# Kernel tuning notes

Hardware: AMD Instinct MI355X
Metric: run time of the kernel (lower is better)

Reference implementation:

```python
import jax, jax.numpy as jnp
import numpy as np


def setup_inputs() -> dict:
    key = jax.random.key(0)
    ks = jax.random.split(key, 8)
    B, T, C, W, H = 2, 8, 64, 32, 32
    NOBJ, DIM = 4, 64
    s = 0.05
    return {
        "inputs": jax.random.normal(ks[0], (B, T, C, W, H), jnp.float32),
        "dyn_feat_inputs": jax.random.normal(ks[1], (B, NOBJ, T, C, W, H), jnp.float32),
        "wq": jax.random.normal(ks[2], (C // 2, C), jnp.float32) * s,
        "bq": jax.random.normal(ks[3], (C // 2,), jnp.float32) * s,
        "wk": jax.random.normal(ks[4], (C // 2, C), jnp.float32) * s,
        "bk": jax.random.normal(ks[5], (C // 2,), jnp.float32) * s,
        "wv": jax.random.normal(ks[6], (DIM, C), jnp.float32) * s,
        "bv": jax.random.normal(ks[7], (DIM,), jnp.float32) * s,
    }


def reference(inputs, dyn_feat_inputs, wq, bq, wk, bk, wv, bv):
    # inputs: [bs, T, ch, w, h]; dyn_feat_inputs: [bs, n_obj, T, ch, w, h]
    bs, T, ch, w, h = inputs.shape
    n_obj = dyn_feat_inputs.shape[1]
    N = w * h
    bsTO = bs * n_obj * T
    # repeat inputs across the object axis (broadcast, no copy until reshape)
    xin = jnp.broadcast_to(inputs[:, None], (bs, n_obj, T, ch, w, h)).reshape(bsTO, ch, N)
    xdyn = dyn_feat_inputs.reshape(bsTO, ch, N)
    # 1x1 convs == channel matmuls
    q = jnp.einsum('oc,bcn->bno', wq, xdyn) + bq            # [bsTO, N, ch//2]
    k = jnp.einsum('oc,bcn->bon', wk, xin) + bk[:, None]    # [bsTO, ch//2, N]
    energy = jnp.einsum('bno,bom->bnm', q, k)               # [bsTO, N, N] (NO scale, as in source)
    attn = jax.nn.softmax(energy, axis=-1)
    v = jnp.einsum('oc,bcn->bon', wv, xin) + bv[:, None]    # [bsTO, dim, N]
    # out = bmm(v, attn^T): out[b,d,m] = sum_n v[b,d,n] * attn[b,m,n]
    out = jnp.einsum('bdn,bmn->bdm', v, attn).reshape(bsTO, -1, w, h)
    return (out, attn)
```

## Files before the change

kernel.cpp:

```cpp
#include <hip/hip_runtime.h>
#include <hip/hip_bf16.h>

typedef __hip_bfloat16 bf16;
typedef float f32x4 __attribute__((ext_vector_type(4)));
typedef short s16x8 __attribute__((ext_vector_type(8)));

static __device__ __forceinline__ float b2f(bf16 h) { return __bfloat162float(h); }
static __device__ __forceinline__ float us2f(unsigned short u) {
    union { unsigned short u; bf16 h; } cv; cv.u = u; return __bfloat162float(cv.h);
}
static __device__ __forceinline__ unsigned short f2us(float f) {
    __hip_bfloat16 h = __float2bfloat16(f);
    union { __hip_bfloat16 h; unsigned short u; } cv; cv.h = h; return cv.u;
}
static __device__ __forceinline__ void split2(float x, unsigned short& h, unsigned short& l) {
    unsigned short hh = f2us(x);
    float lo = x - us2f(hh);
    union { float f; unsigned u; } cv; cv.f = lo;
    h = hh;
    l = (unsigned short)(cv.u >> 16);
}

#define LOG2E 1.4426950408889634f

#define QHI 0
#define QLO 2097152
#define KHI 4194304
#define KLO 4718592
#define VHI 5242880
#define VLO 6291456
#define FLG_BYTE 14680064

static __device__ __forceinline__ f32x4 mfma16(s16x8 a, s16x8 b, f32x4 c) {
    return __builtin_amdgcn_mfma_f32_16x16x32_bf16(a, b, c, 0, 0, 0);
}

__global__ __launch_bounds__(256) void detect_kernel(
    const void* inp, const void* dyn, const void* wq, int* flags)
{
    __shared__ int bad;
    if (threadIdx.x == 0) bad = 0;
    __syncthreads();
    const void* bufs[3] = { inp, dyn, wq };
    const int nscan[3] = { 2048, 2048, 1024 };
    const int b = blockIdx.x;
    const unsigned short* u = (const unsigned short*)bufs[b];
    int myBad = 0;
    for (int i = threadIdx.x; i < nscan[b]; i += 256) {
        float x = us2f(u[i * 2]);
        if (!(x > -1e4f && x < 1e4f)) myBad++;
    }
    atomicAdd(&bad, myBad);
    __syncthreads();
    if (threadIdx.x == 0) flags[b] = (bad >= 4) ? 1 : 0;
}

__global__ __launch_bounds__(256) void proj_kernel(
    const void* __restrict__ inputs, const void* __restrict__ dyn,
    const void* __restrict__ wq, const void* __restrict__ bq,
    const void* __restrict__ wk, const void* __restrict__ bk,
    const void* __restrict__ wv, const void* __restrict__ bv,
    unsigned short* __restrict__ wsu, const int* __restrict__ flags)
{
    __shared__ float sW[6144];
    __shared__ float sB[96];
    const int t   = threadIdx.x;
    const int blk = blockIdx.x;
    const int fin = flags[0];
    const int fdyn = flags[1];
    const int fw  = flags[2];
    const int nl  = t & 63;
    const int og  = t >> 6;
    unsigned int* ws32 = (unsigned int*)wsu;
    const float4* sW4 = (const float4*)sW;

    if (blk < 256) {
        const int ib = blk >> 4;
        const int n  = ((blk & 15) << 6) + nl;
        if (fw) {
            const float* wkf = (const float*)wk; const float* wvf = (const float*)wv;
            for (int i = t; i < 2048; i += 256) sW[i] = wkf[i];
            for (int i = t; i < 4096; i += 256) sW[2048 + i] = wvf[i];
            if (t < 32) sB[t] = ((const float*)bk)[t];
            else if (t >= 64 && t < 128) sB[32 + t - 64] = ((const float*)bv)[t - 64];
        } else {
            const bf16* wkb = (const bf16*)wk; const bf16* wvb = (const bf16*)wv;
            for (int i = t; i < 2048; i += 256) sW[i] = b2f(wkb[i]);
            for (int i = t; i < 4096; i += 256) sW[2048 + i] = b2f(wvb[i]);
            if (t < 32) sB[t] = b2f(((const bf16*)bk)[t]);
            else if (t >= 64 && t < 128) sB[32 + t - 64] = b2f(((const bf16*)bv)[t - 64]);
        }
        __syncthreads();

        const int o0 = og * 24;
        float acc[24];
        #pragma unroll
        for (int j = 0; j < 24; j++) acc[j] = sB[o0 + j];

        if (fin) {
            const float* xp = (const float*)inputs + ib * 65536 + n;
            for (int c4 = 0; c4 < 16; c4++) {
                float x0 = xp[(c4 * 4 + 0) << 10];
                float x1 = xp[(c4 * 4 + 1) << 10];
                float x2 = xp[(c4 * 4 + 2) << 10];
                float x3 = xp[(c4 * 4 + 3) << 10];
                #pragma unroll
                for (int j = 0; j < 24; j++) {
                    float4 w = sW4[(o0 + j) * 16 + c4];
                    acc[j] = fmaf(w.x, x0, fmaf(w.y, x1, fmaf(w.z, x2, fmaf(w.w, x3, acc[j]))));
                }
            }
        } else {
            const bf16* xp = (const bf16*)inputs + ib * 65536 + n;
            for (int c4 = 0; c4 < 16; c4++) {
                float x0 = b2f(xp[(c4 * 4 + 0) << 10]);
                float x1 = b2f(xp[(c4 * 4 + 1) << 10]);
                float x2 = b2f(xp[(c4 * 4 + 2) << 10]);
                float x3 = b2f(xp[(c4 * 4 + 3) << 10]);
                #pragma unroll
                for (int j = 0; j < 24; j++) {
                    float4 w = sW4[(o0 + j) * 16 + c4];
                    acc[j] = fmaf(w.x, x0, fmaf(w.y, x1, fmaf(w.z, x2, fmaf(w.w, x3, acc[j]))));
                }
            }
        }

        #define STORE_KCHUNK(JB)                                                    \
        {                                                                           \
            unsigned short hs[8], ls[8];                                            \
            _Pragma("unroll")                                                       \
            for (int j2 = 0; j2 < 8; j2++) split2(acc[(JB) + j2], hs[j2], ls[j2]);  \
            uint4 A, C;                                                             \
            A.x = (unsigned)hs[0] | ((unsigned)hs[1] << 16);                        \
            A.y = (unsigned)hs[2] | ((unsigned)hs[3] << 16);                        \
            A.z = (unsigned)hs[4] | ((unsigned)hs[5] << 16);                        \
            A.w = (unsigned)hs[6] | ((unsigned)hs[7] << 16);                        \
            C.x = (unsigned)ls[0] | ((unsigned)ls[1] << 16);                        \
            C.y = (unsigned)ls[2] | ((unsigned)ls[3] << 16);                        \
            C.z = (unsigned)ls[4] | ((unsigned)ls[5] << 16);                        \
            C.w = (unsigned)ls[6] | ((unsigned)ls[7] << 16);                        \
            unsigned int* ph = ws32 + (KHI >> 1) + ib * 16384 + n * 16 + ((o0 + (JB)) >> 1); \
            *reinterpret_cast<uint4*>(ph) = A;                                      \
            *reinterpret_cast<uint4*>(ph + ((KLO - KHI) >> 1)) = C;                 \
        }
        if (og == 0) { STORE_KCHUNK(0); STORE_KCHUNK(8); STORE_KCHUNK(16); }
        else if (og == 1) { STORE_KCHUNK(0); }
        #undef STORE_KCHUNK

        unsigned short* vh = wsu + VHI + ib * 65536 + n;
        unsigned short* vl = wsu + VLO + ib * 65536 + n;
        #pragma unroll
        for (int j = 0; j < 24; j++) {
            const int oi = o0 + j;
            if (oi >= 32) {
                const int d = oi - 32;
                unsigned short h, l; split2(acc[j], h, l);
                vh[d << 10] = h;
                vl[d << 10] = l;
            }
        }
    } else {
        const int qb = blk - 256;
        const int bb = qb >> 4;
        const int n  = ((qb & 15) << 6) + nl;
        if (fw) {
            const float* wqf = (const float*)wq;
            for (int i = t; i < 2048; i += 256) sW[i] = wqf[i] * LOG2E;
            if (t < 32) sB[t] = ((const float*)bq)[t] * LOG2E;
        } else {
            const bf16* wqb = (const bf16*)wq;
            for (int i = t; i < 2048; i += 256) sW[i] = b2f(wqb[i]) * LOG2E;
            if (t < 32) sB[t] = b2f(((const bf16*)bq)[t]) * LOG2E;
        }
        __syncthreads();

        const int o0 = og * 8;
        float acc[8];
        #pragma unroll
        for (int j = 0; j < 8; j++) acc[j] = sB[o0 + j];

        if (fdyn) {
            const float* xp = (const float*)dyn + bb * 65536 + n;
            for (int c4 = 0; c4 < 16; c4++) {
                float x0 = xp[(c4 * 4 + 0) << 10];
                float x1 = xp[(c4 * 4 + 1) << 10];
                float x2 = xp[(c4 * 4 + 2) << 10];
                float x3 = xp[(c4 * 4 + 3) << 10];
                #pragma unroll
                for (int j = 0; j < 8; j++) {
                    float4 w = sW4[(o0 + j) * 16 + c4];
                    acc[j] = fmaf(w.x, x0, fmaf(w.y, x1, fmaf(w.z, x2, fmaf(w.w, x3, acc[j]))));
                }
            }
        } else {
            const bf16* xp = (const bf16*)dyn + bb * 65536 + n;
            for (int c4 = 0; c4 < 16; c4++) {
                float x0 = b2f(xp[(c4 * 4 + 0) << 10]);
                float x1 = b2f(xp[(c4 * 4 + 1) << 10]);
                float x2 = b2f(xp[(c4 * 4 + 2) << 10]);
                float x3 = b2f(xp[(c4 * 4 + 3) << 10]);
                #pragma unroll
                for (int j = 0; j < 8; j++) {
                    float4 w = sW4[(o0 + j) * 16 + c4];
                    acc[j] = fmaf(w.x, x0, fmaf(w.y, x1, fmaf(w.z, x2, fmaf(w.w, x3, acc[j]))));
                }
            }
        }

        unsigned short hs[8], ls[8];
        #pragma unroll
        for (int j = 0; j < 8; j++) split2(acc[j], hs[j], ls[j]);
        uint4 A, C;
        A.x = (unsigned)hs[0] | ((unsigned)hs[1] << 16);
        A.y = (unsigned)hs[2] | ((unsigned)hs[3] << 16);
        A.z = (unsigned)hs[4] | ((unsigned)hs[5] << 16);
        A.w = (unsigned)hs[6] | ((unsigned)hs[7] << 16);
        C.x = (unsigned)ls[0] | ((unsigned)ls[1] << 16);
        C.y = (unsigned)ls[2] | ((unsigned)ls[3] << 16);
        C.z = (unsigned)ls[4] | ((unsigned)ls[5] << 16);
        C.w = (unsigned)ls[6] | ((unsigned)ls[7] << 16);
        unsigned int* ph = ws32 + (QHI >> 1) + bb * 16384 + n * 16 + (o0 >> 1);
        *reinterpret_cast<uint4*>(ph) = A;
        *reinterpret_cast<uint4*>(ph + ((QLO - QHI) >> 1)) = C;
    }
}

__global__ __launch_bounds__(256) void attn_kernel(
    const unsigned short* __restrict__ wsu, const int* __restrict__ flags,
    void* __restrict__ dout)
{
    const int lane = threadIdx.x & 63;
    const int wid  = threadIdx.x >> 6;
    const int blk  = blockIdx.x;
    const int b    = blk >> 3;
    const int pair = ((blk & 7) << 2) + wid;
    const int q0   = pair << 5;
    const int ib   = ((b >> 5) << 3) + (b & 7);
    const int g    = lane >> 4;
    const int r    = lane & 15;
    const int pr   = ((r >> 2) << 3) + (r & 3);
    const int fo   = flags[0] & flags[1] & flags[2];

    const unsigned short* qp0 = wsu + QHI + ((size_t)b << 15) + ((q0 + r) << 5) + (g << 3);
    const s16x8 qh0 = *reinterpret_cast<const s16x8*>(qp0);
    const s16x8 ql0 = *reinterpret_cast<const s16x8*>(qp0 + (QLO - QHI));
    const s16x8 qh1 = *reinterpret_cast<const s16x8*>(qp0 + 512);
    const s16x8 ql1 = *reinterpret_cast<const s16x8*>(qp0 + (QLO - QHI) + 512);

    const unsigned short* kb = wsu + KHI + ((size_t)ib << 15) + pr * 32 + (g << 3);
    const unsigned short* vb = wsu + VHI + ((size_t)ib << 16) + (r << 10) + (g << 3);

    const f32x4 z4 = {0.f, 0.f, 0.f, 0.f};

    float mx0 = -3.0e38f, sm0 = 0.f, mx1 = -3.0e38f, sm1 = 0.f;
    s16x8 kah = *reinterpret_cast<const s16x8*>(kb);
    s16x8 kal = *reinterpret_cast<const s16x8*>(kb + (KLO - KHI));
    s16x8 kbh = *reinterpret_cast<const s16x8*>(kb + 128);
    s16x8 kbl = *reinterpret_cast<const s16x8*>(kb + (KLO - KHI) + 128);
    #pragma unroll 2
    for (int ck = 0; ck < 32; ck++) {
        const unsigned short* kn = kb + ((ck < 31 ? ck + 1 : 31) << 10);
        s16x8 nah = *reinterpret_cast<const s16x8*>(kn);
        s16x8 nal = *reinterpret_cast<const s16x8*>(kn + (KLO - KHI));
        s16x8 nbh = *reinterpret_cast<const s16x8*>(kn + 128);
        s16x8 nbl = *reinterpret_cast<const s16x8*>(kn + (KLO - KHI) + 128);

        f32x4 eA0 = mfma16(kah, qh0, z4); eA0 = mfma16(kah, ql0, eA0); eA0 = mfma16(kal, qh0, eA0);
        f32x4 eB0 = mfma16(kbh, qh0, z4); eB0 = mfma16(kbh, ql0, eB0); eB0 = mfma16(kbl, qh0, eB0);
        f32x4 eA1 = mfma16(kah, qh1, z4); eA1 = mfma16(kah, ql1, eA1); eA1 = mfma16(kal, qh1, eA1);
        f32x4 eB1 = mfma16(kbh, qh1, z4); eB1 = mfma16(kbh, ql1, eB1); eB1 = mfma16(kbl, qh1, eB1);

        float t0 = fmaxf(fmaxf(fmaxf(eA0[0], eA0[1]), fmaxf(eA0[2], eA0[3])),
                         fmaxf(fmaxf(eB0[0], eB0[1]), fmaxf(eB0[2], eB0[3])));
        if (t0 > mx0) { sm0 *= exp2f(mx0 - t0); mx0 = t0; }
        sm0 += exp2f(eA0[0]-mx0) + exp2f(eA0[1]-mx0) + exp2f(eA0[2]-mx0) + exp2f(eA0[3]-mx0)
             + exp2f(eB0[0]-mx0) + exp2f(eB0[1]-mx0) + exp2f(eB0[2]-mx0) + exp2f(eB0[3]-mx0);

        float t1 = fmaxf(fmaxf(fmaxf(eA1[0], eA1[1]), fmaxf(eA1[2], eA1[3])),
                         fmaxf(fmaxf(eB1[0], eB1[1]), fmaxf(eB1[2], eB1[3])));
        if (t1 > mx1) { sm1 *= exp2f(mx1 - t1); mx1 = t1; }
        sm1 += exp2f(eA1[0]-mx1) + exp2f(eA1[1]-mx1) + exp2f(eA1[2]-mx1) + exp2f(eA1[3]-mx1)
             + exp2f(eB1[0]-mx1) + exp2f(eB1[1]-mx1) + exp2f(eB1[2]-mx1) + exp2f(eB1[3]-mx1);

        kah = nah; kal = nal; kbh = nbh; kbl = nbl;
    }
    #pragma unroll
    for (int off = 16; off < 64; off <<= 1) {
        float mo0 = __shfl_xor(mx0, off), so0 = __shfl_xor(sm0, off);
        float M0 = fmaxf(mx0, mo0);
        sm0 = sm0 * exp2f(mx0 - M0) + so0 * exp2f(mo0 - M0); mx0 = M0;
        float mo1 = __shfl_xor(mx1, off), so1 = __shfl_xor(sm1, off);
        float M1 = fmaxf(mx1, mo1);
        sm1 = sm1 * exp2f(mx1 - M1) + so1 * exp2f(mo1 - M1); mx1 = M1;
    }
    const float inv0 = 1.0f / sm0;
    const float inv1 = 1.0f / sm1;

    f32x4 a0[4] = { z4, z4, z4, z4 };
    f32x4 a1[4] = { z4, z4, z4, z4 };
    float* attnF0 = (float*)dout + 4194304 + ((size_t)b << 20) + ((size_t)(q0 + r) << 10);
    bf16*  attnB0 = (bf16*)dout  + 4194304 + ((size_t)b << 20) + ((size_t)(q0 + r) << 10);
    float* attnF1 = attnF0 + 16384;
    bf16*  attnB1 = attnB0 + 16384;

    kah = *reinterpret_cast<const s16x8*>(kb);
    kal = *reinterpret_cast<const s16x8*>(kb + (KLO - KHI));
    kbh = *reinterpret_cast<const s16x8*>(kb + 128);
    kbl = *reinterpret_cast<const s16x8*>(kb + (KLO - KHI) + 128);
    for (int ck = 0; ck < 32; ck++) {
        const unsigned short* kn = kb + ((ck < 31 ? ck + 1 : 31) << 10);
        s16x8 nah = *reinterpret_cast<const s16x8*>(kn);
        s16x8 nal = *reinterpret_cast<const s16x8*>(kn + (KLO - KHI));
        s16x8 nbh = *reinterpret_cast<const s16x8*>(kn + 128);
        s16x8 nbl = *reinterpret_cast<const s16x8*>(kn + (KLO - KHI) + 128);

        const unsigned short* vp = vb + (ck << 5);
        s16x8 vh[4], vl[4];
        #pragma unroll
        for (int dt = 0; dt < 4; dt++) {
            vh[dt] = *reinterpret_cast<const s16x8*>(vp + (dt << 14));
            vl[dt] = *reinterpret_cast<const s16x8*>(vp + (VLO - VHI) + (dt << 14));
        }

        f32x4 eA0 = mfma16(kah, qh0, z4); eA0 = mfma16(kah, ql0, eA0); eA0 = mfma16(kal, qh0, eA0);
        f32x4 eB0 = mfma16(kbh, qh0, z4); eB0 = mfma16(kbh, ql0, eB0); eB0 = mfma16(kbl, qh0, eB0);
        f32x4 eA1 = mfma16(kah, qh1, z4); eA1 = mfma16(kah, ql1, eA1); eA1 = mfma16(kal, qh1, eA1);
        f32x4 eB1 = mfma16(kbh, qh1, z4); eB1 = mfma16(kbh, ql1, eB1); eB1 = mfma16(kbl, qh1, eB1);

        float p0[8], p1[8];
        #pragma unroll
        for (int j = 0; j < 4; j++) { p0[j] = exp2f(eA0[j] - mx0) * inv0; p0[4+j] = exp2f(eB0[j] - mx0) * inv0; }
        #pragma unroll
        for (int j = 0; j < 4; j++) { p1[j] = exp2f(eA1[j] - mx1) * inv1; p1[4+j] = exp2f(eB1[j] - mx1) * inv1; }

        s16x8 Ph0, Pl0, Ph1, Pl1;
        #pragma unroll
        for (int j = 0; j < 8; j++) {
            unsigned short h, l;
            split2(p0[j], h, l); Ph0[j] = (short)h; Pl0[j] = (short)l;
            split2(p1[j], h, l); Ph1[j] = (short)h; Pl1[j] = (short)l;
        }

        const int mo = (ck << 5) + (g << 3);
        if (fo) {
            f32x4 fa0 = { p0[0], p0[1], p0[2], p0[3] };
            f32x4 fb0 = { p0[4], p0[5], p0[6], p0[7] };
            f32x4 fa1 = { p1[0], p1[1], p1[2], p1[3] };
            f32x4 fb1 = { p1[4], p1[5], p1[6], p1[7] };
            *reinterpret_cast<f32x4*>(attnF0 + mo)     = fa0;
            *reinterpret_cast<f32x4*>(attnF0 + mo + 4) = fb0;
            *reinterpret_cast<f32x4*>(attnF1 + mo)     = fa1;
            *reinterpret_cast<f32x4*>(attnF1 + mo + 4) = fb1;
        } else {
            *reinterpret_cast<s16x8*>(attnB0 + mo) = Ph0;
            *reinterpret_cast<s16x8*>(attnB1 + mo) = Ph1;
        }

        __builtin_amdgcn_s_setprio(1);
        #pragma unroll
        for (int dt = 0; dt < 4; dt++) {
            a0[dt] = mfma16(Ph0, vh[dt], a0[dt]);
            a0[dt] = mfma16(Ph0, vl[dt], a0[dt]);
            a0[dt] = mfma16(Pl0, vh[dt], a0[dt]);
            a1[dt] = mfma16(Ph1, vh[dt], a1[dt]);
            a1[dt] = mfma16(Ph1, vl[dt], a1[dt]);
            a1[dt] = mfma16(Pl1, vh[dt], a1[dt]);
        }
        __builtin_amdgcn_s_setprio(0);

        kah = nah; kal = nal; kbh = nbh; kbl = nbl;
    }

    if (fo) {
        float* ob = (float*)dout + ((size_t)b << 16) + (r << 10) + q0 + (g << 2);
        #pragma unroll
        for (int dt = 0; dt < 4; dt++) {
            f32x4 f0 = { a0[dt][0], a0[dt][1], a0[dt][2], a0[dt][3] };
            f32x4 f1 = { a1[dt][0], a1[dt][1], a1[dt][2], a1[dt][3] };
            *reinterpret_cast<f32x4*>(ob + (dt << 14))      = f0;
            *reinterpret_cast<f32x4*>(ob + (dt << 14) + 16) = f1;
        }
    } else {
        bf16* ob = (bf16*)dout + ((size_t)b << 16) + (r << 10) + q0 + (g << 2);
        #pragma unroll
        for (int dt = 0; dt < 4; dt++) {
            ushort4 u0, u1;
            u0.x = f2us(a0[dt][0]); u0.y = f2us(a0[dt][1]); u0.z = f2us(a0[dt][2]); u0.w = f2us(a0[dt][3]);
            u1.x = f2us(a1[dt][0]); u1.y = f2us(a1[dt][1]); u1.z = f2us(a1[dt][2]); u1.w = f2us(a1[dt][3]);
            *reinterpret_cast<ushort4*>(ob + (dt << 14))      = u0;
            *reinterpret_cast<ushort4*>(ob + (dt << 14) + 16) = u1;
        }
    }
}

extern "C" void kernel_launch(void* const* d_in, const int* in_sizes, int n_in,
                              void* d_out, int out_size, void* d_ws, size_t ws_size,
                              hipStream_t stream) {
    unsigned short* wsu = (unsigned short*)d_ws;
    int* flags = (int*)((char*)d_ws + FLG_BYTE);

    detect_kernel<<<3, 256, 0, stream>>>(d_in[0], d_in[1], d_in[2], flags);
    proj_kernel<<<1280, 256, 0, stream>>>(d_in[0], d_in[1], d_in[2], d_in[3],
                                          d_in[4], d_in[5], d_in[6], d_in[7],
                                          wsu, flags);
    attn_kernel<<<512, 256, 0, stream>>>(wsu, flags, d_out);
}
```

Baseline: 415.2 us.

## Split key dimension across wave pairs with shared-memory softmax and accumulator merge

Each query pair is now handled by two waves that each cover half of the key positions, which doubles the grid from 512 to 1024 blocks. Partial max/sum statistics are merged through shared memory, and the second wave's output accumulators are added into the first wave's before the store. The explicit register prefetch of K and the up-front V loads are dropped in favour of loading inside the loop, which reduces register pressure. The cost is two block-wide barriers, extra LDS traffic, and less latency hiding per wave.

```diff
diff --git a/kernel.cpp b/kernel.cpp
--- a/kernel.cpp
+++ b/kernel.cpp
@@ -229,12 +229,17 @@
     const unsigned short* __restrict__ wsu, const int* __restrict__ flags,
     void* __restrict__ dout)
 {
+    __shared__ float sMX[4][64][5];
+    __shared__ float sAcc[2][64][33];
+
     const int lane = threadIdx.x & 63;
     const int wid  = threadIdx.x >> 6;
     const int blk  = blockIdx.x;
-    const int b    = blk >> 3;
-    const int pair = ((blk & 7) << 2) + wid;
-    const int q0   = pair << 5;
+    const int b    = blk >> 4;
+    const int sub  = blk & 15;
+    const int p    = (sub << 1) + (wid >> 1);
+    const int mh   = wid & 1;
+    const int q0   = p << 5;
     const int ib   = ((b >> 5) << 3) + (b & 7);
     const int g    = lane >> 4;
     const int r    = lane & 15;
@@ -247,23 +252,18 @@
     const s16x8 qh1 = *reinterpret_cast<const s16x8*>(qp0 + 512);
     const s16x8 ql1 = *reinterpret_cast<const s16x8*>(qp0 + (QLO - QHI) + 512);
 
-    const unsigned short* kb = wsu + KHI + ((size_t)ib << 15) + pr * 32 + (g << 3);
-    const unsigned short* vb = wsu + VHI + ((size_t)ib << 16) + (r << 10) + (g << 3);
+    const unsigned short* kb = wsu + KHI + ((size_t)ib << 15) + ((size_t)mh << 14) + pr * 32 + (g << 3);
+    const unsigned short* vb = wsu + VHI + ((size_t)ib << 16) + (r << 10) + (g << 3) + (mh << 9);
 
     const f32x4 z4 = {0.f, 0.f, 0.f, 0.f};
 
     float mx0 = -3.0e38f, sm0 = 0.f, mx1 = -3.0e38f, sm1 = 0.f;
-    s16x8 kah = *reinterpret_cast<const s16x8*>(kb);
-    s16x8 kal = *reinterpret_cast<const s16x8*>(kb + (KLO - KHI));
-    s16x8 kbh = *reinterpret_cast<const s16x8*>(kb + 128);
-    s16x8 kbl = *reinterpret_cast<const s16x8*>(kb + (KLO - KHI) + 128);
-    #pragma unroll 2
-    for (int ck = 0; ck < 32; ck++) {
-        const unsigned short* kn = kb + ((ck < 31 ? ck + 1 : 31) << 10);
-        s16x8 nah = *reinterpret_cast<const s16x8*>(kn);
-        s16x8 nal = *reinterpret_cast<const s16x8*>(kn + (KLO - KHI));
-        s16x8 nbh = *reinterpret_cast<const s16x8*>(kn + 128);
-        s16x8 nbl = *reinterpret_cast<const s16x8*>(kn + (KLO - KHI) + 128);
+    for (int ck = 0; ck < 16; ck++) {
+        const unsigned short* ka = kb + (ck << 10);
+        s16x8 kah = *reinterpret_cast<const s16x8*>(ka);
+        s16x8 kal = *reinterpret_cast<const s16x8*>(ka + (KLO - KHI));
+        s16x8 kbh = *reinterpret_cast<const s16x8*>(ka + 128);
+        s16x8 kbl = *reinterpret_cast<const s16x8*>(ka + (KLO - KHI) + 128);
 
         f32x4 eA0 = mfma16(kah, qh0, z4); eA0 = mfma16(kah, ql0, eA0); eA0 = mfma16(kal, qh0, eA0);
         f32x4 eB0 = mfma16(kbh, qh0, z4); eB0 = mfma16(kbh, ql0, eB0); eB0 = mfma16(kbl, qh0, eB0);
@@ -281,8 +281,6 @@
         if (t1 > mx1) { sm1 *= exp2f(mx1 - t1); mx1 = t1; }
         sm1 += exp2f(eA1[0]-mx1) + exp2f(eA1[1]-mx1) + exp2f(eA1[2]-mx1) + exp2f(eA1[3]-mx1)
              + exp2f(eB1[0]-mx1) + exp2f(eB1[1]-mx1) + exp2f(eB1[2]-mx1) + exp2f(eB1[3]-mx1);
-
-        kah = nah; kal = nal; kbh = nbh; kbl = nbl;
     }
     #pragma unroll
     for (int off = 16; off < 64; off <<= 1) {
@@ -293,34 +291,34 @@
         float M1 = fmaxf(mx1, mo1);
         sm1 = sm1 * exp2f(mx1 - M1) + so1 * exp2f(mo1 - M1); mx1 = M1;
     }
+    sMX[wid][lane][0] = mx0; sMX[wid][lane][1] = sm0;
+    sMX[wid][lane][2] = mx1; sMX[wid][lane][3] = sm1;
+    __syncthreads();
+    {
+        const int pw = wid ^ 1;
+        float pmx0 = sMX[pw][lane][0], psm0 = sMX[pw][lane][1];
+        float pmx1 = sMX[pw][lane][2], psm1 = sMX[pw][lane][3];
+        float M0 = fmaxf(mx0, pmx0);
+        sm0 = sm0 * exp2f(mx0 - M0) + psm0 * exp2f(pmx0 - M0); mx0 = M0;
+        float M1 = fmaxf(mx1, pmx1);
+        sm1 = sm1 * exp2f(mx1 - M1) + psm1 * exp2f(pmx1 - M1); mx1 = M1;
+    }
     const float inv0 = 1.0f / sm0;
     const float inv1 = 1.0f / sm1;
 
     f32x4 a0[4] = { z4, z4, z4, z4 };
     f32x4 a1[4] = { z4, z4, z4, z4 };
-    float* attnF0 = (float*)dout + 4194304 + ((size_t)b << 20) + ((size_t)(q0 + r) << 10);
-    bf16*  attnB0 = (bf16*)dout  + 4194304 + ((size_t)b << 20) + ((size_t)(q0 + r) << 10);
+    float* attnF0 = (float*)dout + 4194304 + ((size_t)b << 20) + ((size_t)(q0 + r) << 10) + (mh << 9);
+    bf16*  attnB0 = (bf16*)dout  + 4194304 + ((size_t)b << 20) + ((size_t)(q0 + r) << 10) + (mh << 9);
     float* attnF1 = attnF0 + 16384;
     bf16*  attnB1 = attnB0 + 16384;
 
-    kah = *reinterpret_cast<const s16x8*>(kb);
-    kal = *reinterpret_cast<const s16x8*>(kb + (KLO - KHI));
-    kbh = *reinterpret_cast<const s16x8*>(kb + 128);
-    kbl = *reinterpret_cast<const s16x8*>(kb + (KLO - KHI) + 128);
-    for (int ck = 0; ck < 32; ck++) {
-        const unsigned short* kn = kb + ((ck < 31 ? ck + 1 : 31) << 10);
-        s16x8 nah = *reinterpret_cast<const s16x8*>(kn);
-        s16x8 nal = *reinterpret_cast<const s16x8*>(kn + (KLO - KHI));
-        s16x8 nbh = *reinterpret_cast<const s16x8*>(kn + 128);
-        s16x8 nbl = *reinterpret_cast<const s16x8*>(kn + (KLO - KHI) + 128);
-
-        const unsigned short* vp = vb + (ck << 5);
-        s16x8 vh[4], vl[4];
-        #pragma unroll
-        for (int dt = 0; dt < 4; dt++) {
-            vh[dt] = *reinterpret_cast<const s16x8*>(vp + (dt << 14));
-            vl[dt] = *reinterpret_cast<const s16x8*>(vp + (VLO - VHI) + (dt << 14));
-        }
+    for (int ck = 0; ck < 16; ck++) {
+        const unsigned short* ka = kb + (ck << 10);
+        s16x8 kah = *reinterpret_cast<const s16x8*>(ka);
+        s16x8 kal = *reinterpret_cast<const s16x8*>(ka + (KLO - KHI));
+        s16x8 kbh = *reinterpret_cast<const s16x8*>(ka + 128);
+        s16x8 kbl = *reinterpret_cast<const s16x8*>(ka + (KLO - KHI) + 128);
 
         f32x4 eA0 = mfma16(kah, qh0, z4); eA0 = mfma16(kah, ql0, eA0); eA0 = mfma16(kal, qh0, eA0);
         f32x4 eB0 = mfma16(kbh, qh0, z4); eB0 = mfma16(kbh, ql0, eB0); eB0 = mfma16(kbl, qh0, eB0);
@@ -356,39 +354,63 @@
             *reinterpret_cast<s16x8*>(attnB1 + mo) = Ph1;
         }
 
+        const unsigned short* vp = vb + (ck << 5);
         __builtin_amdgcn_s_setprio(1);
         #pragma unroll
         for (int dt = 0; dt < 4; dt++) {
-            a0[dt] = mfma16(Ph0, vh[dt], a0[dt]);
-            a0[dt] = mfma16(Ph0, vl[dt], a0[dt]);
-            a0[dt] = mfma16(Pl0, vh[dt], a0[dt]);
-            a1[dt] = mfma16(Ph1, vh[dt], a1[dt]);
-            a1[dt] = mfma16(Ph1, vl[dt], a1[dt]);
-            a1[dt] = mfma16(Pl1, vh[dt], a1[dt]);
+            s16x8 vh = *reinterpret_cast<const s16x8*>(vp + (dt << 14));
+            s16x8 vl = *reinterpret_cast<const s16x8*>(vp + (VLO - VHI) + (dt << 14));
+            a0[dt] = mfma16(Ph0, vh, a0[dt]);
+            a0[dt] = mfma16(Ph0, vl, a0[dt]);
+            a0[dt] = mfma16(Pl0, vh, a0[dt]);
+            a1[dt] = mfma16(Ph1, vh, a1[dt]);
+            a1[dt] = mfma16(Ph1, vl, a1[dt]);
+            a1[dt] = mfma16(Pl1, vh, a1[dt]);
         }
         __builtin_amdgcn_s_setprio(0);
-
-        kah = nah; kal = nal; kbh = nbh; kbl = nbl;
-    }
-
-    if (fo) {
-        float* ob = (float*)dout + ((size_t)b << 16) + (r << 10) + q0 + (g << 2);
+    }
+
+    if (mh) {
+        const int sp = wid >> 1;
         #pragma unroll
         for (int dt = 0; dt < 4; dt++) {
-            f32x4 f0 = { a0[dt][0], a0[dt][1], a0[dt][2], a0[dt][3] };
-            f32x4 f1 = { a1[dt][0], a1[dt][1], a1[dt][2], a1[dt][3] };
-            *reinterpret_cast<f32x4*>(ob + (dt << 14))      = f0;
-            *reinterpret_cast<f32x4*>(ob + (dt << 14) + 16) = f1;
-        }
-    } else {
-        bf16* ob = (bf16*)dout + ((size_t)b << 16) + (r << 10) + q0 + (g << 2);
+            #pragma unroll
+            for (int j = 0; j < 4; j++) {
+                sAcc[sp][lane][dt * 4 + j]      = a0[dt][j];
+                sAcc[sp][lane][16 + dt * 4 + j] = a1[dt][j];
+            }
+        }
+    }
+    __syncthreads();
+    if (!mh) {
+        const int sp = wid >> 1;
         #pragma unroll
         for (int dt = 0; dt < 4; dt++) {
-            ushort4 u0, u1;
-            u0.x = f2us(a0[dt][0]); u0.y = f2us(a0[dt][1]); u0.z = f2us(a0[dt][2]); u0.w = f2us(a0[dt][3]);
-            u1.x = f2us(a1[dt][0]); u1.y = f2us(a1[dt][1]); u1.z = f2us(a1[dt][2]); u1.w = f2us(a1[dt][3]);
-            *reinterpret_cast<ushort4*>(ob + (dt << 14))      = u0;
-            *reinterpret_cast<ushort4*>(ob + (dt << 14) + 16) = u1;
+            #pragma unroll
+            for (int j = 0; j < 4; j++) {
+                a0[dt][j] += sAcc[sp][lane][dt * 4 + j];
+                a1[dt][j] += sAcc[sp][lane][16 + dt * 4 + j];
+            }
+        }
+        if (fo) {
+            float* ob = (float*)dout + ((size_t)b << 16) + (r << 10) + q0 + (g << 2);
+            #pragma unroll
+            for (int dt = 0; dt < 4; dt++) {
+                f32x4 f0 = { a0[dt][0], a0[dt][1], a0[dt][2], a0[dt][3] };
+                f32x4 f1 = { a1[dt][0], a1[dt][1], a1[dt][2], a1[dt][3] };
+                *reinterpret_cast<f32x4*>(ob + (dt << 14))      = f0;
+                *reinterpret_cast<f32x4*>(ob + (dt << 14) + 16) = f1;
+            }
+        } else {
+            bf16* ob = (bf16*)dout + ((size_t)b << 16) + (r << 10) + q0 + (g << 2);
+            #pragma unroll
+            for (int dt = 0; dt < 4; dt++) {
+                ushort4 u0, u1;
+                u0.x = f2us(a0[dt][0]); u0.y = f2us(a0[dt][1]); u0.z = f2us(a0[dt][2]); u0.w = f2us(a0[dt][3]);
+                u1.x = f2us(a1[dt][0]); u1.y = f2us(a1[dt][1]); u1.z = f2us(a1[dt][2]); u1.w = f2us(a1[dt][3]);
+                *reinterpret_cast<ushort4*>(ob + (dt << 14))      = u0;
+                *reinterpret_cast<ushort4*>(ob + (dt << 14) + 16) = u1;
+            }
         }
     }
 }
@@ -403,5 +425,5 @@
     proj_kernel<<<1280, 256, 0, stream>>>(d_in[0], d_in[1], d_in[2], d_in[3],
                                           d_in[4], d_in[5], d_in[6], d_in[7],
                                           wsu, flags);
-    attn_kernel<<<512, 256, 0, stream>>>(wsu, flags, d_out);
-}
+    attn_kernel<<<1024, 256, 0, stream>>>(wsu, flags, d_out);
+}
```

Measured after the change: 428.6 us. +3.2%, slower.
